# Kernel tuning notes

Hardware: AMD Instinct MI355X
Metric: run time of the kernel (lower is better)

## Reference

```python
import jax, jax.numpy as jnp
import numpy as np

B, S, DIN, DH, HN, CHUNK = 8, 8192, 512, 512, 4, 16
HD = DH // HN
LN_EPS = 1e-5
CLAMP = 1e-6


def setup_inputs() -> dict:
    key = jax.random.key(0)
    ks = jax.random.split(key, 8)
    x = jax.random.normal(ks[0], (B, S, DIN), jnp.float32)
    h = jax.random.normal(ks[1], (B, DH), jnp.float32)
    s_in = 1.0 / np.sqrt(DIN)
    W_in = jax.random.uniform(ks[2], (DH, DIN), jnp.float32, -s_in, s_in)
    ln_gamma = jnp.ones((DH,), jnp.float32)
    ln_beta = jnp.zeros((DH,), jnp.float32)
    s_h = 1.0 / np.sqrt(DH)
    W_gate = jax.random.uniform(ks[3], (2 * HN, DH), jnp.float32, -s_h, s_h)
    b_gate = jax.random.uniform(ks[4], (2 * HN,), jnp.float32, -s_h, s_h)
    # raw = atanh(0.9) as in _init_eigenvalues
    eig_raw = jnp.full((HN,), 0.5 * np.log(1.9 / 0.1), jnp.float32)
    W_out = jax.random.uniform(ks[5], (DH, DH), jnp.float32, -s_h, s_h)
    return {"x": x, "h": h, "W_in": W_in, "ln_gamma": ln_gamma, "ln_beta": ln_beta,
            "W_gate": W_gate, "b_gate": b_gate, "eig_raw": eig_raw, "W_out": W_out}


def _forward(x, h, W_in, ln_gamma, ln_beta, W_gate, b_gate, eig_raw, W_out):
    # input projection (no bias) + layernorm
    xp = jnp.einsum('bsi,hi->bsh', x, W_in)
    mu = xp.mean(-1, keepdims=True)
    var = xp.var(-1, keepdims=True)  # biased var, matches torch LayerNorm
    xn = (xp - mu) / jnp.sqrt(var + LN_EPS) * ln_gamma + ln_beta
    # gates
    gates = jnp.einsum('bsh,gh->bsg', xn, W_gate) + b_gate
    alpha = jax.nn.sigmoid(gates[..., :HN])   # (B,S,HN)
    beta = jax.nn.sigmoid(gates[..., HN:])    # (B,S,HN)
    eig = jnp.tanh(eig_raw)                   # (HN,)
    a = eig[None, None, :] * alpha            # (B,S,HN)
    xh = xn.reshape(B, S, HN, HD)
    b = beta[..., None] * xh                  # (B,S,HN,HD)
    h0 = h.reshape(B, HN, HD)
    # chunked parallel scan: h_t = a_t * h_{t-1} + b_t
    nc = S // CHUNK
    a_c = a.reshape(B, nc, CHUNK, HN).transpose(1, 0, 2, 3)          # (nc,B,C,HN)
    b_c = b.reshape(B, nc, CHUNK, HN, HD).transpose(1, 0, 2, 3, 4)   # (nc,B,C,HN,HD)

    def step(hc, ab):
        ac, bc = ab
        cum_a = jnp.cumprod(ac, axis=1)                      # (B,C,HN)
        cum_a_safe = jnp.maximum(cum_a, CLAMP)[..., None]    # clamp(min=1e-6)
        first = cum_a[..., None] * hc[:, None]               # (B,C,HN,HD)
        second = cum_a_safe * jnp.cumsum(bc / cum_a_safe, axis=1)
        h_chunk = first + second
        return h_chunk[:, -1], h_chunk

    _, outs = jax.lax.scan(step, h0, (a_c, b_c))             # outs: (nc,B,C,HN,HD)
    h_all = outs.transpose(1, 0, 2, 3, 4).reshape(B, S, DH)
    out = jnp.einsum('bsh,oh->bso', h_all, W_out)            # dropout is identity (eval)
    return out, h_all[:, -1, :]


def reference(x, h, W_in, ln_gamma, ln_beta, W_gate, b_gate, eig_raw, W_out):
    return _forward(x, h, W_in, ln_gamma, ln_beta, W_gate, b_gate, eig_raw, W_out)
```

## Files before the change

kernel.cpp:

```cpp
#include <hip/hip_runtime.h>
#include <hip/hip_bf16.h>
#include <math.h>

#define B_    8
#define S_    8192
#define DIN_  512
#define DH_   512
#define HN_   4
#define HD_   128
#define CHUNK_ 16
#define NC_   (S_/CHUNK_)
#define NTOK  (B_*S_)

typedef __bf16 bf16x8 __attribute__((ext_vector_type(8)));
typedef float  f32x4  __attribute__((ext_vector_type(4)));

__device__ __forceinline__ float sigmoidf_(float z) { return 1.0f / (1.0f + expf(-z)); }

__device__ __forceinline__ unsigned short f2bf(float f) {
    union { float f; unsigned u; } v; v.f = f;
    unsigned u = v.u;
    u += 0x7fffu + ((u >> 16) & 1u);
    return (unsigned short)(u >> 16);
}
__device__ __forceinline__ float bf2f(unsigned short s) {
    union { unsigned u; float f; } c; c.u = ((unsigned)s) << 16; return c.f;
}
__device__ __forceinline__ unsigned long long pack4bf(float4 a) {
    union { __bf16 h[4]; unsigned long long u; } c;
    c.h[0] = (__bf16)a.x; c.h[1] = (__bf16)a.y;
    c.h[2] = (__bf16)a.z; c.h[3] = (__bf16)a.w;
    return c.u;
}
__device__ __forceinline__ void gload_lds16(const void* g, void* lds) {
    __builtin_amdgcn_global_load_lds(
        (const __attribute__((address_space(1))) unsigned int*)g,
        (__attribute__((address_space(3))) unsigned int*)lds, 16, 0, 0);
}

#define AOFF(og, r) ((((og) << 11) + ((r) << 4)) ^ ((og) << 5))
#define BOFF(og, c) (((og) << 11) + ((c) << 4))

#define XCD_DECODE(mt, ct)                        \
    const int _bid = blockIdx.x;                  \
    const int _j = _bid >> 3;                     \
    const int mt = ((_j >> 2) << 3) + (_bid & 7); \
    const int ct = _j & 3;

__global__ __launch_bounds__(256) void k0_convert(
    const float* __restrict__ Win, const float* __restrict__ Wout,
    unsigned short* __restrict__ WreA, unsigned short* __restrict__ WreB)
{
    int idx = blockIdx.x * 256 + threadIdx.x;
    if (idx < 262144) {
        int c_g = idx >> 9, k = idx & 511;
        int dst = ((((c_g >> 7) * 16 + (k >> 5)) * 4 + ((k >> 3) & 3)) << 10)
                + ((c_g & 127) << 3) + (k & 7);
        WreA[dst] = f2bf(Win[idx]);
        WreB[dst] = f2bf(Wout[idx]);
    }
}

__global__ __launch_bounds__(256) void gemm1(
    const float* __restrict__ x, const unsigned short* __restrict__ Wre,
    unsigned short* __restrict__ xpb)
{
    __shared__ alignas(16) unsigned short Bl[4096];
    __shared__ alignas(16) unsigned short Al[4096];
    char* Blc = (char*)Bl; char* Alc = (char*)Al;
    const int tid = threadIdx.x;
    const int l = tid & 63, wid = tid >> 6;
    const int og = l >> 4, lr = l & 15;
    const int wr = wid >> 1, wc2 = wid & 1;
    XCD_DECODE(mt, ct)
    const long t0 = (long)mt * 128;
    const int c0 = ct << 7;
    const int r0 = tid >> 2, ogk = tid & 3;

    f32x4 acc[4][4];
    #pragma unroll
    for (int m = 0; m < 4; ++m)
        #pragma unroll
        for (int n = 0; n < 4; ++n) acc[m][n] = (f32x4)(0.f);

    for (int kt = 0; kt < 16; ++kt) {
        __syncthreads();
        const char* gB = (const char*)Wre + ((long)(ct * 16 + kt) << 13);
        gload_lds16(gB + (wid << 10) + (l << 4),        Blc + (wid << 10));
        gload_lds16(gB + 4096 + (wid << 10) + (l << 4), Blc + 4096 + (wid << 10));
        const int kb = kt << 5;
        const float* xr0 = &x[(t0 + r0) * 512 + kb + (ogk << 3)];
        const float* xr1 = &x[(t0 + r0 + 64) * 512 + kb + (ogk << 3)];
        float4 a0 = *(const float4*)xr0, a1 = *(const float4*)(xr0 + 4);
        float4 b0 = *(const float4*)xr1, b1 = *(const float4*)(xr1 + 4);
        ulonglong2 w0, w1;
        w0.x = pack4bf(a0); w0.y = pack4bf(a1);
        w1.x = pack4bf(b0); w1.y = pack4bf(b1);
        *(ulonglong2*)(Alc + AOFF(ogk, r0))      = w0;
        *(ulonglong2*)(Alc + AOFF(ogk, r0 + 64)) = w1;
        __syncthreads();

        bf16x8 afr[4], bfr[4];
        #pragma unroll
        for (int m = 0; m < 4; ++m)
            afr[m] = *(const bf16x8*)(Alc + AOFF(og, (wr << 6) + (m << 4) + lr));
        #pragma unroll
        for (int n = 0; n < 4; ++n)
            bfr[n] = *(const bf16x8*)(Blc + BOFF(og, (wc2 << 6) + (n << 4) + lr));
        #pragma unroll
        for (int m = 0; m < 4; ++m)
            #pragma unroll
            for (int n = 0; n < 4; ++n)
                acc[m][n] = __builtin_amdgcn_mfma_f32_16x16x32_bf16(afr[m], bfr[n], acc[m][n], 0, 0, 0);
    }

    #pragma unroll
    for (int m = 0; m < 4; ++m) {
        const long rb = t0 + (wr << 6) + (m << 4) + (og << 2);
        #pragma unroll
        for (int n = 0; n < 4; ++n) {
            const int col = c0 + (wc2 << 6) + (n << 4) + lr;
            #pragma unroll
            for (int j = 0; j < 4; ++j)
                xpb[(rb + j) * 512 + col] = f2bf(acc[m][n][j]);
        }
    }
}

__global__ __launch_bounds__(256) void k_lnA(
    const unsigned short* __restrict__ xpb,
    const float* __restrict__ gamma, const float* __restrict__ beta,
    const float* __restrict__ Wg, const float* __restrict__ bg,
    const float* __restrict__ eig_raw,
    unsigned short* __restrict__ A2, float* __restrict__ B15,
    float* __restrict__ p_buf)
{
    __shared__ float bnS[16][512];
    __shared__ float WgL[8][512];
    __shared__ float qS[16][4];
    __shared__ float rqS[16][4];
    __shared__ float aS[16][4];

    const int tid = threadIdx.x;
    const int l = tid & 63, w = tid >> 6;
    const int lg = l >> 4;
    const int li = l & 15;
    const int r  = (w << 2) + lg;
    const long t0 = (long)blockIdx.x * 16;
    const long tok = t0 + r;

    float4 v[8];
    #pragma unroll
    for (int jj = 0; jj < 8; ++jj) {
        const ushort4 u = *(const ushort4*)&xpb[tok * 512 + (jj << 6) + (li << 2)];
        v[jj] = make_float4(bf2f(u.x), bf2f(u.y), bf2f(u.z), bf2f(u.w));
    }

    #pragma unroll
    for (int i = 0; i < 4; ++i)
        ((float4*)WgL)[tid + 256 * i] = ((const float4*)Wg)[tid + 256 * i];
    __syncthreads();

    float s1 = 0.f, s2 = 0.f;
    #pragma unroll
    for (int jj = 0; jj < 8; ++jj) {
        s1 += v[jj].x + v[jj].y + v[jj].z + v[jj].w;
        s2 += v[jj].x*v[jj].x + v[jj].y*v[jj].y + v[jj].z*v[jj].z + v[jj].w*v[jj].w;
    }
    #pragma unroll
    for (int o = 1; o < 16; o <<= 1) { s1 += __shfl_xor(s1, o, 64); s2 += __shfl_xor(s2, o, 64); }
    const float mean = s1 * (1.f/512.f);
    const float var  = s2 * (1.f/512.f) - mean*mean;
    const float rstd = 1.0f / sqrtf(var + 1e-5f);

    #pragma unroll
    for (int jj = 0; jj < 8; ++jj) {
        const float4 g = *(const float4*)&gamma[(jj << 6) + (li << 2)];
        const float4 b = *(const float4*)&beta[(jj << 6) + (li << 2)];
        v[jj].x = (v[jj].x - mean)*rstd*g.x + b.x;
        v[jj].y = (v[jj].y - mean)*rstd*g.y + b.y;
        v[jj].z = (v[jj].z - mean)*rstd*g.z + b.z;
        v[jj].w = (v[jj].w - mean)*rstd*g.w + b.w;
    }

    float gt[8];
    #pragma unroll
    for (int g = 0; g < 8; ++g) {
        float p = 0.f;
        #pragma unroll
        for (int jj = 0; jj < 8; ++jj) {
            const float4 wv = *(const float4*)&WgL[g][(jj << 6) + (li << 2)];
            p = fmaf(v[jj].x, wv.x, p); p = fmaf(v[jj].y, wv.y, p);
            p = fmaf(v[jj].z, wv.z, p); p = fmaf(v[jj].w, wv.w, p);
        }
        #pragma unroll
        for (int o = 1; o < 16; o <<= 1) p += __shfl_xor(p, o, 64);
        gt[g] = p + bg[g];
    }

    const float bt[4] = {sigmoidf_(gt[4]), sigmoidf_(gt[5]), sigmoidf_(gt[6]), sigmoidf_(gt[7])};
    #pragma unroll
    for (int jj = 0; jj < 8; ++jj) {
        const float b = bt[jj >> 1];
        *(float4*)&bnS[r][(jj << 6) + (li << 2)] =
            make_float4(b*v[jj].x, b*v[jj].y, b*v[jj].z, b*v[jj].w);
    }
    if (li < 4) aS[r][li] = tanhf(eig_raw[li]) * sigmoidf_(gt[li]);
    __syncthreads();

    if (tid < 4) {
        const int n = tid;
        float p = 1.f;
        #pragma unroll
        for (int t = 0; t < 16; ++t) {
            p *= aS[t][n];
            p_buf[(t0 + t) * 4 + n] = p;
            const float q = fmaxf(p, 1e-6f);
            qS[t][n] = q;
            rqS[t][n] = 1.0f / q;
        }
    }
    __syncthreads();

    #pragma unroll
    for (int cc = 0; cc < 2; ++cc) {
        const int c = tid + (cc << 8);
        const int n = c >> 7;
        float s = 0.f;
        #pragma unroll
        for (int t = 0; t < 16; ++t) {
            s = fmaf(bnS[t][c], rqS[t][n], s);
            const float vv = qS[t][n] * s;
            bnS[t][c] = vv;
            if (t == 15) B15[blockIdx.x * 512 + c] = vv;
        }
    }
    __syncthreads();

    const long mtb = t0 >> 7;
    #pragma unroll
    for (int i = 0; i < 4; ++i) {
        const int slot = (i << 8) + tid;
        const int t = slot >> 6, oct = slot & 63;
        const float4 va = *(const float4*)&bnS[t][oct << 3];
        const float4 vb = *(const float4*)&bnS[t][(oct << 3) + 4];
        const int rr = (int)((t0 + t) & 127);
        const long idx = (((mtb * 16 + (oct >> 2)) * 4 + (oct & 3)) << 10) + (rr << 3);
        ulonglong2 wv; wv.x = pack4bf(va); wv.y = pack4bf(vb);
        *(ulonglong2*)&A2[idx] = wv;
    }
}

__global__ __launch_bounds__(256) void k3_scan(
    const float* __restrict__ p_buf, const float* __restrict__ B15,
    const float* __restrict__ h_in, float* __restrict__ h0_buf,
    float* __restrict__ h_last)
{
    const int tid = blockIdx.x * blockDim.x + threadIdx.x;
    const int b = tid >> 9, c = tid & 511, n = c >> 7;
    float h = h_in[b * DH_ + c];
    for (int ch = 0; ch < NC_; ++ch) {
        const long gc = b * NC_ + ch;
        h0_buf[gc * 512 + c] = h;
        const long sE = (long)b * S_ + (long)ch * CHUNK_ + (CHUNK_ - 1);
        h = fmaf(p_buf[sE * HN_ + n], h, B15[gc * 512 + c]);
    }
    h_last[b * DH_ + c] = h;
}

__global__ __launch_bounds__(256) void kG(
    const float* __restrict__ h0, const unsigned short* __restrict__ Wre,
    float* __restrict__ G)
{
    __shared__ alignas(16) unsigned short Bl[4096];
    __shared__ alignas(16) unsigned short Al[4096];
    char* Blc = (char*)Bl; char* Alc = (char*)Al;
    const int tid = threadIdx.x;
    const int l = tid & 63, wid = tid >> 6;
    const int og = l >> 4, lr = l & 15;
    const int wr = wid >> 1, wc2 = wid & 1;
    const int ct = blockIdx.x & 3, mt = (blockIdx.x >> 2) & 31, hn = blockIdx.x >> 7;
    const long g0 = (long)mt * 128;
    const int c0 = ct << 7;
    const int r0 = tid >> 2, ogk = tid & 3;

    f32x4 acc[4][4];
    #pragma unroll
    for (int m = 0; m < 4; ++m)
        #pragma unroll
        for (int n = 0; n < 4; ++n) acc[m][n] = (f32x4)(0.f);

    for (int s = 0; s < 4; ++s) {
        const int kt = (hn << 2) + s;
        __syncthreads();
        const char* gB = (const char*)Wre + ((long)(ct * 16 + kt) << 13);
        gload_lds16(gB + (wid << 10) + (l << 4),        Blc + (wid << 10));
        gload_lds16(gB + 4096 + (wid << 10) + (l << 4), Blc + 4096 + (wid << 10));
        const int kb = (hn << 7) + (s << 5);
        const float* xr0 = &h0[(g0 + r0) * 512 + kb + (ogk << 3)];
        const float* xr1 = &h0[(g0 + r0 + 64) * 512 + kb + (ogk << 3)];
        float4 a0 = *(const float4*)xr0, a1 = *(const float4*)(xr0 + 4);
        float4 b0 = *(const float4*)xr1, b1 = *(const float4*)(xr1 + 4);
        ulonglong2 w0, w1;
        w0.x = pack4bf(a0); w0.y = pack4bf(a1);
        w1.x = pack4bf(b0); w1.y = pack4bf(b1);
        *(ulonglong2*)(Alc + AOFF(ogk, r0))      = w0;
        *(ulonglong2*)(Alc + AOFF(ogk, r0 + 64)) = w1;
        __syncthreads();

        bf16x8 afr[4], bfr[4];
        #pragma unroll
        for (int m = 0; m < 4; ++m)
            afr[m] = *(const bf16x8*)(Alc + AOFF(og, (wr << 6) + (m << 4) + lr));
        #pragma unroll
        for (int n = 0; n < 4; ++n)
            bfr[n] = *(const bf16x8*)(Blc + BOFF(og, (wc2 << 6) + (n << 4) + lr));
        #pragma unroll
        for (int m = 0; m < 4; ++m)
            #pragma unroll
            for (int n = 0; n < 4; ++n)
                acc[m][n] = __builtin_amdgcn_mfma_f32_16x16x32_bf16(afr[m], bfr[n], acc[m][n], 0, 0, 0);
    }

    float* Gh = G + ((long)hn << 21);
    #pragma unroll
    for (int m = 0; m < 4; ++m) {
        const long rb = g0 + (wr << 6) + (m << 4) + (og << 2);
        #pragma unroll
        for (int n = 0; n < 4; ++n) {
            const int col = c0 + (wc2 << 6) + (n << 4) + lr;
            #pragma unroll
            for (int j = 0; j < 4; ++j)
                Gh[(rb + j) * 512 + col] = acc[m][n][j];
        }
    }
}

__global__ __launch_bounds__(256) void gemm2(
    const unsigned short* __restrict__ A2, const unsigned short* __restrict__ Wre,
    const float* __restrict__ G, const float* __restrict__ p_buf,
    float* __restrict__ out)
{
    __shared__ alignas(16) unsigned short Bl[4096];
    __shared__ alignas(16) unsigned short Al[4096];
    __shared__ float pS[512];
    char* Blc = (char*)Bl; char* Alc = (char*)Al;
    const int tid = threadIdx.x;
    const int l = tid & 63, wid = tid >> 6;
    const int og = l >> 4, lr = l & 15;
    const int wr = wid >> 1, wc2 = wid & 1;
    XCD_DECODE(mt, ct)
    const long t0 = (long)mt * 128;
    const int c0 = ct << 7;

    pS[tid]       = p_buf[t0 * 4 + tid];
    pS[tid + 256] = p_buf[t0 * 4 + 256 + tid];

    f32x4 acc[4][4];
    #pragma unroll
    for (int m = 0; m < 4; ++m)
        #pragma unroll
        for (int n = 0; n < 4; ++n) acc[m][n] = (f32x4)(0.f);

    for (int kt = 0; kt < 16; ++kt) {
        __syncthreads();
        const char* gB = (const char*)Wre + ((long)(ct * 16 + kt) << 13);
        gload_lds16(gB + (wid << 10) + (l << 4),        Blc + (wid << 10));
        gload_lds16(gB + 4096 + (wid << 10) + (l << 4), Blc + 4096 + (wid << 10));
        const char* gA = (const char*)A2 + ((long)(mt * 16 + kt) << 13);
        gload_lds16(gA + (wid << 10) + (l << 4),        Alc + (wid << 10));
        gload_lds16(gA + 4096 + (wid << 10) + (l << 4), Alc + 4096 + (wid << 10));
        __syncthreads();

        bf16x8 afr[4], bfr[4];
        #pragma unroll
        for (int m = 0; m < 4; ++m)
            afr[m] = *(const bf16x8*)(Alc + BOFF(og, (wr << 6) + (m << 4) + lr));
        #pragma unroll
        for (int n = 0; n < 4; ++n)
            bfr[n] = *(const bf16x8*)(Blc + BOFF(og, (wc2 << 6) + (n << 4) + lr));
        #pragma unroll
        for (int m = 0; m < 4; ++m)
            #pragma unroll
            for (int n = 0; n < 4; ++n)
                acc[m][n] = __builtin_amdgcn_mfma_f32_16x16x32_bf16(afr[m], bfr[n], acc[m][n], 0, 0, 0);
    }

    #pragma unroll
    for (int m = 0; m < 4; ++m) {
        const long gcm = (t0 >> 4) + (wr << 2) + m;
        #pragma unroll
        for (int n = 0; n < 4; ++n) {
            const int col = c0 + (wc2 << 6) + (n << 4) + lr;
            const float g0v = G[gcm * 512 + col];
            const float g1v = G[(1L << 21) + gcm * 512 + col];
            const float g2v = G[(2L << 21) + gcm * 512 + col];
            const float g3v = G[(3L << 21) + gcm * 512 + col];
            #pragma unroll
            for (int j = 0; j < 4; ++j) {
                const int rl = (wr << 6) + (m << 4) + (og << 2) + j;
                const float add = pS[rl*4]*g0v + pS[rl*4+1]*g1v + pS[rl*4+2]*g2v + pS[rl*4+3]*g3v;
                out[(t0 + rl) * 512 + col] = acc[m][n][j] + add;
            }
        }
    }
}

extern "C" void kernel_launch(void* const* d_in, const int* in_sizes, int n_in,
                              void* d_out, int out_size, void* d_ws, size_t ws_size,
                              hipStream_t stream) {
    const float* x       = (const float*)d_in[0];
    const float* h       = (const float*)d_in[1];
    const float* Win     = (const float*)d_in[2];
    const float* gamma   = (const float*)d_in[3];
    const float* beta    = (const float*)d_in[4];
    const float* Wg      = (const float*)d_in[5];
    const float* bg      = (const float*)d_in[6];
    const float* eig_raw = (const float*)d_in[7];
    const float* Wout    = (const float*)d_in[8];

    float* out    = (float*)d_out;
    float* h_last = out + (long)NTOK * DH_;
    unsigned short* xpb = (unsigned short*)d_out;

    float* ws     = (float*)d_ws;
    float* p_buf  = ws;
    float* h0_buf = ws + 262144;
    float* B15    = ws + 2359296;
    float* G      = ws + 4456448;
    unsigned short* WreA = (unsigned short*)(ws + 12845056);
    unsigned short* WreB = WreA + 262144;
    unsigned short* A2   = (unsigned short*)(ws + 13107200);

    k0_convert<<<1024, 256, 0, stream>>>(Win, Wout, WreA, WreB);
    gemm1<<<2048, 256, 0, stream>>>(x, WreA, xpb);
    k_lnA<<<NTOK/16, 256, 0, stream>>>(xpb, gamma, beta, Wg, bg, eig_raw,
                                       A2, B15, p_buf);
    k3_scan<<<16, 256, 0, stream>>>(p_buf, B15, h, h0_buf, h_last);
    kG<<<512, 256, 0, stream>>>(h0_buf, WreB, G);
    gemm2<<<2048, 256, 0, stream>>>(A2, WreB, G, p_buf, out);
}
```

Measured before the change: 251.6 us.

## Split sequential inter-chunk scan into compose, short scan, and expand passes

The single-pass inter-chunk recurrence ran on only 16 blocks, with each thread walking 512 dependent chunk steps. It is replaced by a three-level scan. First, 512 blocks compose groups of 16 chunks into (P,Q) affine pairs. Then 16 blocks scan the 32 groups per batch, and finally 512 blocks expand the group-start states back to per-chunk h0. This shortens the serial latency chain at the cost of two extra kernel launches and rereading p_buf and B15. The G buffer is reused as scratch before kG overwrites it.

```diff
diff --git a/kernel.cpp b/kernel.cpp
--- a/kernel.cpp
+++ b/kernel.cpp
@@ -251,21 +251,60 @@
     }
 }
 
-__global__ __launch_bounds__(256) void k3_scan(
+__global__ __launch_bounds__(256) void k3a_compose(
     const float* __restrict__ p_buf, const float* __restrict__ B15,
-    const float* __restrict__ h_in, float* __restrict__ h0_buf,
+    float* __restrict__ Pg, float* __restrict__ Qg)
+{
+    const int gid = blockIdx.x * 256 + threadIdx.x;
+    const int c = gid & 511, g = (gid >> 9) & 31, b = gid >> 14;
+    const int n = c >> 7;
+    float P = 1.f, Q = 0.f;
+    #pragma unroll
+    for (int j = 0; j < 16; ++j) {
+        const int ch = (g << 4) + j;
+        const long gc = (long)b * NC_ + ch;
+        const long sE = (long)b * S_ + (long)ch * CHUNK_ + (CHUNK_ - 1);
+        const float p15 = p_buf[sE * HN_ + n];
+        const float b15 = B15[gc * 512 + c];
+        P *= p15;
+        Q = fmaf(p15, Q, b15);
+    }
+    Pg[(long)gid] = P;
+    Qg[(long)gid] = Q;
+}
+
+__global__ __launch_bounds__(256) void k3b_scan(
+    const float* __restrict__ Pg, const float* __restrict__ Qg,
+    const float* __restrict__ h_in, float* __restrict__ h0g,
     float* __restrict__ h_last)
 {
     const int tid = blockIdx.x * blockDim.x + threadIdx.x;
-    const int b = tid >> 9, c = tid & 511, n = c >> 7;
+    const int b = tid >> 9, c = tid & 511;
     float h = h_in[b * DH_ + c];
-    for (int ch = 0; ch < NC_; ++ch) {
-        const long gc = b * NC_ + ch;
+    for (int g = 0; g < 32; ++g) {
+        const long i = ((long)(b * 32 + g)) * 512 + c;
+        h0g[i] = h;
+        h = fmaf(Pg[i], h, Qg[i]);
+    }
+    h_last[b * DH_ + c] = h;
+}
+
+__global__ __launch_bounds__(256) void k3c_expand(
+    const float* __restrict__ p_buf, const float* __restrict__ B15,
+    const float* __restrict__ h0g, float* __restrict__ h0_buf)
+{
+    const int gid = blockIdx.x * 256 + threadIdx.x;
+    const int c = gid & 511, g = (gid >> 9) & 31, b = gid >> 14;
+    const int n = c >> 7;
+    float h = h0g[(long)gid];
+    #pragma unroll
+    for (int j = 0; j < 16; ++j) {
+        const int ch = (g << 4) + j;
+        const long gc = (long)b * NC_ + ch;
         h0_buf[gc * 512 + c] = h;
         const long sE = (long)b * S_ + (long)ch * CHUNK_ + (CHUNK_ - 1);
         h = fmaf(p_buf[sE * HN_ + n], h, B15[gc * 512 + c]);
     }
-    h_last[b * DH_ + c] = h;
 }
 
 __global__ __launch_bounds__(256) void kG(
@@ -432,11 +471,17 @@
     unsigned short* WreB = WreA + 262144;
     unsigned short* A2   = (unsigned short*)(ws + 13107200);
 
+    float* Pg  = G;
+    float* Qg  = G + 131072;
+    float* h0g = G + 262144;
+
     k0_convert<<<1024, 256, 0, stream>>>(Win, Wout, WreA, WreB);
     gemm1<<<2048, 256, 0, stream>>>(x, WreA, xpb);
     k_lnA<<<NTOK/16, 256, 0, stream>>>(xpb, gamma, beta, Wg, bg, eig_raw,
                                        A2, B15, p_buf);
-    k3_scan<<<16, 256, 0, stream>>>(p_buf, B15, h, h0_buf, h_last);
+    k3a_compose<<<512, 256, 0, stream>>>(p_buf, B15, Pg, Qg);
+    k3b_scan<<<16, 256, 0, stream>>>(Pg, Qg, h, h0g, h_last);
+    k3c_expand<<<512, 256, 0, stream>>>(p_buf, B15, h0g, h0_buf);
     kG<<<512, 256, 0, stream>>>(h0_buf, WreB, G);
     gemm2<<<2048, 256, 0, stream>>>(A2, WreB, G, p_buf, out);
 }
```

Result: faster. 223.1 us (-11.3%).
